# Kernel optimization log

Hardware: AMD Instinct MI355X
Metric: run time of the kernel (lower is better)

## Reference

```python
import jax, jax.numpy as jnp
import numpy as np

B, S_SRC, S_TGT = 32, 64, 1024
D, H, DFF, LE, LD, V = 128, 8, 512, 6, 6, 64


def _pe(S, d):
    # PyTorch-style sinusoidal positional encoding, shape [S, d]
    pos = np.arange(S, dtype=np.float32)[:, None]
    div = np.exp(np.arange(0, d, 2, dtype=np.float32) * (-np.log(10000.0) / d))
    pe = np.zeros((S, d), dtype=np.float32)
    pe[:, 0::2] = np.sin(pos * div)
    pe[:, 1::2] = np.cos(pos * div)
    return jnp.asarray(pe)


def _ln(x, g, b, eps=1e-5):
    m = x.mean(-1, keepdims=True)
    v = ((x - m) ** 2).mean(-1, keepdims=True)
    return (x - m) / jnp.sqrt(v + eps) * g + b


def _mha(q_in, k_in, v_in, Wqkv, bqkv, Wo, bo):
    d = q_in.shape[-1]
    dh = d // H
    def proj(x, W, b):
        return (x @ W.T + b).reshape(x.shape[0], x.shape[1], H, dh)
    q = proj(q_in, Wqkv[:d], bqkv[:d])
    k = proj(k_in, Wqkv[d:2 * d], bqkv[d:2 * d])
    v = proj(v_in, Wqkv[2 * d:], bqkv[2 * d:])
    scores = jnp.einsum('bqhd,bkhd->bhqk', q, k) * (1.0 / np.sqrt(dh))
    a = jax.nn.softmax(scores, axis=-1)
    o = jnp.einsum('bhqk,bkhd->bqhd', a, v).reshape(q_in.shape[0], q_in.shape[1], d)
    return o @ Wo.T + bo


def _ffn(x, W1, b1, W2, b2):
    return jax.nn.relu(x @ W1.T + b1) @ W2.T + b2


def reference(src, tgt, emb,
              enc_qkv_w, enc_qkv_b, enc_out_w, enc_out_b,
              enc_ln1_g, enc_ln1_b, enc_ff1_w, enc_ff1_b,
              enc_ff2_w, enc_ff2_b, enc_ln2_g, enc_ln2_b,
              enc_norm_g, enc_norm_b,
              dec_sa_qkv_w, dec_sa_qkv_b, dec_sa_out_w, dec_sa_out_b,
              dec_ln1_g, dec_ln1_b,
              dec_ca_qkv_w, dec_ca_qkv_b, dec_ca_out_w, dec_ca_out_b,
              dec_ln2_g, dec_ln2_b,
              dec_ff1_w, dec_ff1_b, dec_ff2_w, dec_ff2_b,
              dec_ln3_g, dec_ln3_b, dec_norm_g, dec_norm_b,
              fc_w, fc_b):
    # src: [B, S_SRC] int tokens (occupation config); tgt: [B, S_TGT, D] (zeros in the original)
    s = emb[src] * np.sqrt(float(D)) + _pe(src.shape[1], D)
    t = tgt + _pe(tgt.shape[1], D)
    # encoder (post-norm, ReLU, dropout=0 in eval)
    for i in range(LE):
        s = _ln(s + _mha(s, s, s, enc_qkv_w[i], enc_qkv_b[i], enc_out_w[i], enc_out_b[i]),
                enc_ln1_g[i], enc_ln1_b[i])
        s = _ln(s + _ffn(s, enc_ff1_w[i], enc_ff1_b[i], enc_ff2_w[i], enc_ff2_b[i]),
                enc_ln2_g[i], enc_ln2_b[i])
    mem = _ln(s, enc_norm_g, enc_norm_b)
    # decoder
    for i in range(LD):
        t = _ln(t + _mha(t, t, t, dec_sa_qkv_w[i], dec_sa_qkv_b[i], dec_sa_out_w[i], dec_sa_out_b[i]),
                dec_ln1_g[i], dec_ln1_b[i])
        t = _ln(t + _mha(t, mem, mem, dec_ca_qkv_w[i], dec_ca_qkv_b[i], dec_ca_out_w[i], dec_ca_out_b[i]),
                dec_ln2_g[i], dec_ln2_b[i])
        t = _ln(t + _ffn(t, dec_ff1_w[i], dec_ff1_b[i], dec_ff2_w[i], dec_ff2_b[i]),
                dec_ln3_g[i], dec_ln3_b[i])
    t = _ln(t, dec_norm_g, dec_norm_b)
    return t @ fc_w.T + fc_b  # [B, S_TGT, 1] transformer correction to TN params


def setup_inputs():
    ks = iter(jax.random.split(jax.random.key(0), 64))
    def nrm(shape, scale=0.02):
        return jax.random.normal(next(ks), shape, dtype=jnp.float32) * scale
    inp = {
        'src': jax.random.randint(next(ks), (B, S_SRC), 0, V),
        'tgt': jnp.zeros((B, S_TGT, D), jnp.float32),
        'emb': nrm((V, D), 1.0),
        'enc_qkv_w': nrm((LE, 3 * D, D)), 'enc_qkv_b': jnp.zeros((LE, 3 * D)),
        'enc_out_w': nrm((LE, D, D)), 'enc_out_b': jnp.zeros((LE, D)),
        'enc_ln1_g': jnp.ones((LE, D)), 'enc_ln1_b': jnp.zeros((LE, D)),
        'enc_ff1_w': nrm((LE, DFF, D)), 'enc_ff1_b': jnp.zeros((LE, DFF)),
        'enc_ff2_w': nrm((LE, D, DFF)), 'enc_ff2_b': jnp.zeros((LE, D)),
        'enc_ln2_g': jnp.ones((LE, D)), 'enc_ln2_b': jnp.zeros((LE, D)),
        'enc_norm_g': jnp.ones((D,)), 'enc_norm_b': jnp.zeros((D,)),
        'dec_sa_qkv_w': nrm((LD, 3 * D, D)), 'dec_sa_qkv_b': jnp.zeros((LD, 3 * D)),
        'dec_sa_out_w': nrm((LD, D, D)), 'dec_sa_out_b': jnp.zeros((LD, D)),
        'dec_ln1_g': jnp.ones((LD, D)), 'dec_ln1_b': jnp.zeros((LD, D)),
        'dec_ca_qkv_w': nrm((LD, 3 * D, D)), 'dec_ca_qkv_b': jnp.zeros((LD, 3 * D)),
        'dec_ca_out_w': nrm((LD, D, D)), 'dec_ca_out_b': jnp.zeros((LD, D)),
        'dec_ln2_g': jnp.ones((LD, D)), 'dec_ln2_b': jnp.zeros((LD, D)),
        'dec_ff1_w': nrm((LD, DFF, D)), 'dec_ff1_b': jnp.zeros((LD, DFF)),
        'dec_ff2_w': nrm((LD, D, DFF)), 'dec_ff2_b': jnp.zeros((LD, D)),
        'dec_ln3_g': jnp.ones((LD, D)), 'dec_ln3_b': jnp.zeros((LD, D)),
        'dec_norm_g': jnp.ones((D,)), 'dec_norm_b': jnp.zeros((D,)),
        'fc_w': nrm((1, D)), 'fc_b': jnp.zeros((1,)),
    }
    return inp
```

## Files before the change

kernel.cpp:

```cpp
#include <hip/hip_runtime.h>
#include <hip/hip_bf16.h>
#include <stdint.h>

#define NH 8

typedef uint16_t u16;
typedef uint32_t u32;
typedef __attribute__((ext_vector_type(8))) short s8b;
typedef __attribute__((ext_vector_type(4))) float f32x4;
typedef __attribute__((ext_vector_type(16))) float f32x16;

#if __has_builtin(__builtin_amdgcn_exp2f)
#define EXPS(x) __builtin_amdgcn_exp2f(x)
#define QSCALE 0.36067376022224085f
#else
#define EXPS(x) __expf(x)
#define QSCALE 0.25f
#endif

__device__ __forceinline__ u16 f2b(float f) {
    u32 u = __builtin_bit_cast(u32, f);
    u = (u + 0x7fffu + ((u >> 16) & 1u)) >> 16;
    return (u16)u;
}

__device__ __forceinline__ u32 pkbf(float a, float b) {
    u32 ua = __builtin_bit_cast(u32, a) + 0x8000u;
    u32 ub = __builtin_bit_cast(u32, b) + 0x8000u;
    return __builtin_amdgcn_perm(ub, ua, 0x07060302);
}

__device__ __forceinline__ float pe_val(int pos, int d) {
    int j = d >> 1;
    float div = expf((float)j * -0.14391156831212787f);
    float ang = (float)pos * div;
    return (d & 1) ? cosf(ang) : sinf(ang);
}

__global__ void embed_kernel(const int* __restrict__ src, const float* __restrict__ emb,
                             float* __restrict__ S, u16* __restrict__ Sb) {
    int idx = blockIdx.x * 256 + threadIdx.x;
    int d = idx & 127;
    int n = idx >> 7;
    int i = n & 63;
    int tok = src[n];
    float v = emb[tok * 128 + d] * 11.313708498984761f + pe_val(i, d);
    S[idx] = v; Sb[idx] = f2b(v);
}

__global__ void addpe_kernel(const float* __restrict__ tgt, float* __restrict__ T,
                             u16* __restrict__ Tb) {
    int idx = blockIdx.x * 256 + threadIdx.x;
    int d = idx & 127;
    int n = idx >> 7;
    int i = n & 1023;
    float v = tgt[idx] + pe_val(i, d);
    T[idx] = v; Tb[idx] = f2b(v);
}

struct CvtJobs { const float* src[10]; u16* dst[10]; int n[10]; };
__global__ void cvt_kernel(CvtJobs jb) {
    int e = blockIdx.y;
    int i = blockIdx.x * 256 + threadIdx.x;
    if (i < jb.n[e]) jb.dst[e][i] = f2b(jb.src[e][i]);
}

template <int AI, int BJ, int WM, int WN, int RELU>
__global__ __launch_bounds__(64 * WM * WN) void gemm_direct(
    const u16* __restrict__ A, const u16* __restrict__ W,
    const float* __restrict__ bias, u16* __restrict__ C,
    int M, int N, int K, float qscale, int qcols,
    u16* __restrict__ vt, int vcol0, int sshift, int smask, int skv) {
    int tid = threadIdx.x;
    int lane = tid & 63, w = tid >> 6;
    int quad = lane >> 4, l15 = lane & 15;
    int wmi = w % WM, wni = w / WM;
    int m0 = blockIdx.y * (16 * AI * WM), n0 = blockIdx.x * (16 * BJ * WN);
    int mb = m0 + wmi * 16 * AI, nb = n0 + wni * 16 * BJ;

    const u16* Ab = A + (size_t)(mb + l15) * K + quad * 8;
    const u16* Wb = W + (size_t)(nb + l15) * K + quad * 8;

    f32x4 acc[AI][BJ];
#pragma unroll
    for (int i = 0; i < AI; i++)
#pragma unroll
        for (int j = 0; j < BJ; j++)
#pragma unroll
            for (int r = 0; r < 4; r++) acc[i][j][r] = 0.f;

#pragma unroll 2
    for (int k0 = 0; k0 < K; k0 += 32) {
        s8b af[AI], bf[BJ];
#pragma unroll
        for (int i = 0; i < AI; i++) af[i] = *(const s8b*)(Ab + (size_t)16 * i * K + k0);
#pragma unroll
        for (int j = 0; j < BJ; j++) bf[j] = *(const s8b*)(Wb + (size_t)16 * j * K + k0);
#pragma unroll
        for (int i = 0; i < AI; i++)
#pragma unroll
            for (int j = 0; j < BJ; j++)
                acc[i][j] = __builtin_amdgcn_mfma_f32_16x16x32_bf16(af[i], bf[j], acc[i][j], 0, 0, 0);
    }

    if (vt && n0 == vcol0) {
#pragma unroll
        for (int j = 0; j < BJ; j++) {
            int lc = wni * 16 * BJ + 16 * j + l15;
            int h = lc >> 4, n = lc & 15;
            float bv = bias[vcol0 + lc];
#pragma unroll
            for (int i = 0; i < AI; i++) {
                int row = mb + 16 * i + quad * 4;
                int b = row >> sshift, tok = row & smask;
                u32 lo = pkbf(acc[i][j][0] + bv, acc[i][j][1] + bv);
                u32 hi = pkbf(acc[i][j][2] + bv, acc[i][j][3] + bv);
                u32* p = (u32*)(vt + ((size_t)((b * 8 + h) * 16 + n)) * skv + tok);
                p[0] = lo; p[1] = hi;
            }
        }
        return;
    }
#pragma unroll
    for (int j = 0; j < BJ; j++) {
        int col = nb + 16 * j + l15;
        float bv = bias[col];
        float sc = (col < qcols) ? qscale : 1.f;
#pragma unroll
        for (int i = 0; i < AI; i++) {
            int rbase = mb + 16 * i + quad * 4;
#pragma unroll
            for (int r = 0; r < 4; r++) {
                float v = (acc[i][j][r] + bv) * sc;
                if (RELU) v = fmaxf(v, 0.f);
                C[(size_t)(rbase + r) * N + col] = f2b(v);
            }
        }
    }
}

template <int AI, int BJ, int WM, int WN>
__global__ __launch_bounds__(64 * WM * WN) void gemm_ln_t(
    const u16* __restrict__ A, const u16* __restrict__ W,
    const float* __restrict__ bias, const float* __restrict__ X,
    const float* __restrict__ g, const float* __restrict__ bta,
    float* __restrict__ Y, u16* __restrict__ Yb, int M, int K) {
    __shared__ float redS[16 * AI * WM][WN], redQ[16 * AI * WM][WN];
    int tid = threadIdx.x;
    int lane = tid & 63, w = tid >> 6;
    int quad = lane >> 4, l15 = lane & 15;
    int wmi = w % WM, wni = w / WM;
    int m0 = blockIdx.x * (16 * AI * WM);
    int mb = m0 + wmi * 16 * AI, nb = wni * 16 * BJ;

    const u16* Ab = A + (size_t)(mb + l15) * K + quad * 8;
    const u16* Wb = W + (size_t)(nb + l15) * K + quad * 8;

    f32x4 acc[AI][BJ];
#pragma unroll
    for (int i = 0; i < AI; i++)
#pragma unroll
        for (int j = 0; j < BJ; j++)
#pragma unroll
            for (int r = 0; r < 4; r++) acc[i][j][r] = 0.f;

#pragma unroll 2
    for (int k0 = 0; k0 < K; k0 += 32) {
        s8b af[AI], bf[BJ];
#pragma unroll
        for (int i = 0; i < AI; i++) af[i] = *(const s8b*)(Ab + (size_t)16 * i * K + k0);
#pragma unroll
        for (int j = 0; j < BJ; j++) bf[j] = *(const s8b*)(Wb + (size_t)16 * j * K + k0);
#pragma unroll
        for (int i = 0; i < AI; i++)
#pragma unroll
            for (int j = 0; j < BJ; j++)
                acc[i][j] = __builtin_amdgcn_mfma_f32_16x16x32_bf16(af[i], bf[j], acc[i][j], 0, 0, 0);
    }

#pragma unroll
    for (int i = 0; i < AI; i++)
#pragma unroll
        for (int r = 0; r < 4; r++) {
            int row = mb + 16 * i + quad * 4 + r;
            float s = 0.f, q = 0.f;
#pragma unroll
            for (int j = 0; j < BJ; j++) {
                int col = nb + 16 * j + l15;
                float x = acc[i][j][r] + bias[col] + X[(size_t)row * 128 + col];
                acc[i][j][r] = x;
                s += x; q += x * x;
            }
#pragma unroll
            for (int off = 1; off < 16; off <<= 1) {
                s += __shfl_xor(s, off);
                q += __shfl_xor(q, off);
            }
            if (l15 == 0) {
                int lrow = wmi * 16 * AI + 16 * i + quad * 4 + r;
                redS[lrow][wni] = s;
                redQ[lrow][wni] = q;
            }
        }
    __syncthreads();
#pragma unroll
    for (int i = 0; i < AI; i++)
#pragma unroll
        for (int r = 0; r < 4; r++) {
            int lrow = wmi * 16 * AI + 16 * i + quad * 4 + r;
            int row = m0 + lrow;
            float S2 = 0.f, Q2 = 0.f;
#pragma unroll
            for (int u = 0; u < WN; u++) { S2 += redS[lrow][u]; Q2 += redQ[lrow][u]; }
            float mean = S2 * (1.f / 128.f);
            float var = Q2 * (1.f / 128.f) - mean * mean;
            float rstd = rsqrtf(var + 1e-5f);
#pragma unroll
            for (int j = 0; j < BJ; j++) {
                int col = nb + 16 * j + l15;
                float y = (acc[i][j][r] - mean) * rstd * g[col] + bta[col];
                Y[(size_t)row * 128 + col] = y;
                Yb[(size_t)row * 128 + col] = f2b(y);
            }
        }
}

template <int WAVES>
__global__ __launch_bounds__(WAVES * 64) void attn3(
    const u16* __restrict__ Qb, int qstride, int qoff,
    const u16* __restrict__ Kb, int kstride, int koff,
    const u16* __restrict__ VT,
    u16* __restrict__ O, int SQ, int SKV) {
    __shared__ __align__(16) u32 Ps[WAVES][32 * 20];
    int tid = threadIdx.x;
    int lane = tid & 63, w = tid >> 6;
    int quad = lane >> 4, l15 = lane & 15, l31 = lane & 31, half = lane >> 5;
    int nqc = SQ / (WAVES * 32);
    int bid = blockIdx.x;
    int qc = bid % nqc;
    int h = (bid / nqc) % NH;
    int b = bid / (nqc * NH);
    int q0 = qc * WAVES * 32 + w * 32;

    const u16* qp = Qb + (size_t)(b * SQ + q0 + l31) * qstride + qoff + h * 16 + half * 8;
    s8b qf = *(const s8b*)qp;
    s8b ones;
#pragma unroll
    for (int j = 0; j < 8; j++) ones[j] = (short)0x3F80;

    const u16* vtb = VT + ((size_t)(b * NH + h) * 16 + l15) * SKV + quad * 8;
    const u16* kp = Kb + (size_t)(b * SKV + l31) * kstride + koff + h * 16 + half * 8;
    size_t kadv = (size_t)32 * kstride;

    f32x4 O0, O1, L0, L1;
#pragma unroll
    for (int r = 0; r < 4; r++) { O0[r] = 0.f; O1[r] = 0.f; L0[r] = 0.f; L1[r] = 0.f; }

    u32* pw = Ps[w];
#pragma unroll 2
    for (int j0 = 0; j0 < SKV; j0 += 32) {
        s8b kf = *(const s8b*)kp;
        kp += kadv;
        s8b vb = *(const s8b*)(vtb + j0);
        f32x16 S;
#pragma unroll
        for (int r = 0; r < 16; r++) S[r] = 0.f;
        S = __builtin_amdgcn_mfma_f32_32x32x16_bf16(kf, qf, S, 0, 0, 0);
#pragma unroll
        for (int g = 0; g < 4; g++) {
            float p0 = EXPS(S[4 * g + 0]);
            float p1 = EXPS(S[4 * g + 1]);
            float p2 = EXPS(S[4 * g + 2]);
            float p3 = EXPS(S[4 * g + 3]);
            int kw = l31 * 20 + 2 * half + 4 * g;
            pw[kw] = pkbf(p0, p1);
            pw[kw + 1] = pkbf(p2, p3);
        }
        __builtin_amdgcn_wave_barrier();
        s8b pa0 = *(const s8b*)(pw + l15 * 20 + quad * 4);
        s8b pa1 = *(const s8b*)(pw + (16 + l15) * 20 + quad * 4);
        O0 = __builtin_amdgcn_mfma_f32_16x16x32_bf16(pa0, vb, O0, 0, 0, 0);
        O1 = __builtin_amdgcn_mfma_f32_16x16x32_bf16(pa1, vb, O1, 0, 0, 0);
        L0 = __builtin_amdgcn_mfma_f32_16x16x32_bf16(pa0, ones, L0, 0, 0, 0);
        L1 = __builtin_amdgcn_mfma_f32_16x16x32_bf16(pa1, ones, L1, 0, 0, 0);
    }
#pragma unroll
    for (int r = 0; r < 4; r++) {
        int q = b * SQ + q0 + quad * 4 + r;
        O[(size_t)q * 128 + h * 16 + l15] = f2b(O0[r] / L0[r]);
        O[(size_t)(q + 16) * 128 + h * 16 + l15] = f2b(O1[r] / L1[r]);
    }
}

__global__ void ln_kernel(const float* __restrict__ X, const float* __restrict__ R,
                          const float* __restrict__ g, const float* __restrict__ bta,
                          float* __restrict__ Y, u16* __restrict__ Yb) {
    int r = blockIdx.x;
    int lane = threadIdx.x;
    size_t base = (size_t)r * 128;
    float x0 = X[base + lane], x1 = X[base + lane + 64];
    if (R) { x0 += R[base + lane]; x1 += R[base + lane + 64]; }
    float s = x0 + x1;
    for (int off = 32; off; off >>= 1) s += __shfl_xor(s, off);
    float mean = s * (1.f / 128.f);
    float d0 = x0 - mean, d1 = x1 - mean;
    float vs = d0 * d0 + d1 * d1;
    for (int off = 32; off; off >>= 1) vs += __shfl_xor(vs, off);
    float rstd = rsqrtf(vs * (1.f / 128.f) + 1e-5f);
    float y0 = d0 * rstd * g[lane] + bta[lane];
    float y1 = d1 * rstd * g[lane + 64] + bta[lane + 64];
    Y[base + lane] = y0;
    Y[base + lane + 64] = y1;
    if (Yb) { Yb[base + lane] = f2b(y0); Yb[base + lane + 64] = f2b(y1); }
}

__global__ void fc_kernel(const float* __restrict__ X, const float* __restrict__ w,
                          const float* __restrict__ b, float* __restrict__ out) {
    int r = blockIdx.x;
    int lane = threadIdx.x;
    size_t base = (size_t)r * 128;
    float s = X[base + lane] * w[lane] + X[base + lane + 64] * w[lane + 64];
    for (int off = 32; off; off >>= 1) s += __shfl_xor(s, off);
    if (lane == 0) out[r] = s + b[0];
}

static inline void gemmD(const u16* A, const u16* W, const float* bias, u16* C,
                         int M, int N, int K, hipStream_t st, int qcols = 0,
                         u16* vt = nullptr, int vcol0 = 0, int sshift = 0, int skv = 0) {
    hipLaunchKernelGGL((gemm_direct<4, 4, 2, 2, 0>), dim3(N / 128, M / 128), dim3(256), 0, st,
                       A, W, bias, C, M, N, K, QSCALE, qcols, vt, vcol0, sshift, (1 << sshift) - 1, skv);
}
static inline void gemmDr(const u16* A, const u16* W, const float* bias, u16* C,
                          int M, int N, int K, hipStream_t st) {
    hipLaunchKernelGGL((gemm_direct<4, 4, 2, 2, 1>), dim3(N / 128, M / 128), dim3(256), 0, st,
                       A, W, bias, C, M, N, K, 1.f, 0, (u16*)nullptr, 0, 0, 0, 0);
}
static inline void gemmE(const u16* A, const u16* W, const float* bias, u16* C,
                         int M, int N, int K, hipStream_t st, int qcols = 0,
                         u16* vt = nullptr, int vcol0 = 0, int sshift = 0, int skv = 0) {
    hipLaunchKernelGGL((gemm_direct<2, 2, 1, 4, 0>), dim3(N / 128, M / 32), dim3(256), 0, st,
                       A, W, bias, C, M, N, K, QSCALE, qcols, vt, vcol0, sshift, (1 << sshift) - 1, skv);
}
static inline void gemmEr(const u16* A, const u16* W, const float* bias, u16* C,
                          int M, int N, int K, hipStream_t st) {
    hipLaunchKernelGGL((gemm_direct<2, 2, 1, 4, 1>), dim3(N / 128, M / 32), dim3(256), 0, st,
                       A, W, bias, C, M, N, K, 1.f, 0, (u16*)nullptr, 0, 0, 0, 0);
}
static inline void gemmlnD(const u16* A, const u16* W, const float* bias,
                           const float* X, const float* g, const float* bta,
                           float* Y, u16* Yb, int M, int K, hipStream_t st) {
    hipLaunchKernelGGL((gemm_ln_t<4, 4, 2, 2>), dim3(M / 128), dim3(256), 0, st,
                       A, W, bias, X, g, bta, Y, Yb, M, K);
}
static inline void gemmlnE(const u16* A, const u16* W, const float* bias,
                           const float* X, const float* g, const float* bta,
                           float* Y, u16* Yb, int M, int K, hipStream_t st) {
    hipLaunchKernelGGL((gemm_ln_t<2, 2, 1, 4>), dim3(M / 32), dim3(256), 0, st,
                       A, W, bias, X, g, bta, Y, Yb, M, K);
}

extern "C" void kernel_launch(void* const* d_in, const int* in_sizes, int n_in,
                              void* d_out, int out_size, void* d_ws, size_t ws_size,
                              hipStream_t stream) {
    const int B = 32, SSRC = 64, STGT = 1024, D = 128, DFF_ = 512, LE = 6, LD = 6;

    const int*   src = (const int*)d_in[0];
    const float* tgt = (const float*)d_in[1];
    const float* emb = (const float*)d_in[2];
    const float* enc_qkv_w = (const float*)d_in[3];
    const float* enc_qkv_b = (const float*)d_in[4];
    const float* enc_out_w = (const float*)d_in[5];
    const float* enc_out_b = (const float*)d_in[6];
    const float* enc_ln1_g = (const float*)d_in[7];
    const float* enc_ln1_b = (const float*)d_in[8];
    const float* enc_ff1_w = (const float*)d_in[9];
    const float* enc_ff1_b = (const float*)d_in[10];
    const float* enc_ff2_w = (const float*)d_in[11];
    const float* enc_ff2_b = (const float*)d_in[12];
    const float* enc_ln2_g = (const float*)d_in[13];
    const float* enc_ln2_b = (const float*)d_in[14];
    const float* enc_norm_g = (const float*)d_in[15];
    const float* enc_norm_b = (const float*)d_in[16];
    const float* dec_sa_qkv_w = (const float*)d_in[17];
    const float* dec_sa_qkv_b = (const float*)d_in[18];
    const float* dec_sa_out_w = (const float*)d_in[19];
    const float* dec_sa_out_b = (const float*)d_in[20];
    const float* dec_ln1_g = (const float*)d_in[21];
    const float* dec_ln1_b = (const float*)d_in[22];
    const float* dec_ca_qkv_w = (const float*)d_in[23];
    const float* dec_ca_qkv_b = (const float*)d_in[24];
    const float* dec_ca_out_w = (const float*)d_in[25];
    const float* dec_ca_out_b = (const float*)d_in[26];
    const float* dec_ln2_g = (const float*)d_in[27];
    const float* dec_ln2_b = (const float*)d_in[28];
    const float* dec_ff1_w = (const float*)d_in[29];
    const float* dec_ff1_b = (const float*)d_in[30];
    const float* dec_ff2_w = (const float*)d_in[31];
    const float* dec_ff2_b = (const float*)d_in[32];
    const float* dec_ln3_g = (const float*)d_in[33];
    const float* dec_ln3_b = (const float*)d_in[34];
    const float* dec_norm_g = (const float*)d_in[35];
    const float* dec_norm_b = (const float*)d_in[36];
    const float* fc_w = (const float*)d_in[37];
    const float* fc_b = (const float*)d_in[38];

    const int NT = B * STGT;
    const int NS = B * SSRC;

    float* t_f   = (float*)d_ws;
    float* s_f   = t_f + (size_t)NT * D;
    float* mem_f = s_f + (size_t)NS * D;
    u16* t_bf    = (u16*)(mem_f + (size_t)NS * D);
    u16* s_bf    = t_bf + (size_t)NT * D;
    u16* mem_bf  = s_bf + (size_t)NS * D;
    u16* qkv_bf  = mem_bf + (size_t)NS * D;
    u16* attno_bf = qkv_bf + (size_t)NT * DFF_;
    u16* ckv_bf  = attno_bf + (size_t)NT * D;
    u16* vt      = ckv_bf + (size_t)NS * 2 * D;
    u16* wa      = vt + (size_t)B * NH * 16 * STGT;

    u16* w_enc_qkv = wa;                          int n_enc_qkv = LE * 3 * D * D;
    u16* w_enc_out = w_enc_qkv + n_enc_qkv;       int n_enc_out = LE * D * D;
    u16* w_enc_ff1 = w_enc_out + n_enc_out;       int n_enc_ff1 = LE * DFF_ * D;
    u16* w_enc_ff2 = w_enc_ff1 + n_enc_ff1;       int n_enc_ff2 = LE * D * DFF_;
    u16* w_sa_qkv  = w_enc_ff2 + n_enc_ff2;       int n_sa_qkv = LD * 3 * D * D;
    u16* w_sa_out  = w_sa_qkv + n_sa_qkv;         int n_sa_out = LD * D * D;
    u16* w_ca_qkv  = w_sa_out + n_sa_out;         int n_ca_qkv = LD * 3 * D * D;
    u16* w_ca_out  = w_ca_qkv + n_ca_qkv;         int n_ca_out = LD * D * D;
    u16* w_ff1     = w_ca_out + n_ca_out;         int n_ff1 = LD * DFF_ * D;
    u16* w_ff2     = w_ff1 + n_ff1;               int n_ff2 = LD * D * DFF_;

    float* scf = (float*)qkv_bf;

    CvtJobs jb;
    jb.src[0] = enc_qkv_w;    jb.dst[0] = w_enc_qkv; jb.n[0] = n_enc_qkv;
    jb.src[1] = enc_out_w;    jb.dst[1] = w_enc_out; jb.n[1] = n_enc_out;
    jb.src[2] = enc_ff1_w;    jb.dst[2] = w_enc_ff1; jb.n[2] = n_enc_ff1;
    jb.src[3] = enc_ff2_w;    jb.dst[3] = w_enc_ff2; jb.n[3] = n_enc_ff2;
    jb.src[4] = dec_sa_qkv_w; jb.dst[4] = w_sa_qkv;  jb.n[4] = n_sa_qkv;
    jb.src[5] = dec_sa_out_w; jb.dst[5] = w_sa_out;  jb.n[5] = n_sa_out;
    jb.src[6] = dec_ca_qkv_w; jb.dst[6] = w_ca_qkv;  jb.n[6] = n_ca_qkv;
    jb.src[7] = dec_ca_out_w; jb.dst[7] = w_ca_out;  jb.n[7] = n_ca_out;
    jb.src[8] = dec_ff1_w;    jb.dst[8] = w_ff1;     jb.n[8] = n_ff1;
    jb.src[9] = dec_ff2_w;    jb.dst[9] = w_ff2;     jb.n[9] = n_ff2;
    int maxn = n_enc_ff1;
    hipLaunchKernelGGL(cvt_kernel, dim3((maxn + 255) / 256, 10), dim3(256), 0, stream, jb);

    hipLaunchKernelGGL(embed_kernel, dim3(NS * D / 256), dim3(256), 0, stream, src, emb, s_f, s_bf);

    for (int i = 0; i < LE; i++) {
        gemmE(s_bf, w_enc_qkv + (size_t)i * 3 * D * D, enc_qkv_b + (size_t)i * 3 * D,
              qkv_bf, NS, 3 * D, D, stream, 128, vt, 256, 6, SSRC);
        hipLaunchKernelGGL((attn3<2>), dim3(B * NH), dim3(128), 0, stream,
                           qkv_bf, 3 * D, 0, qkv_bf, 3 * D, D, vt, attno_bf, SSRC, SSRC);
        gemmlnE(attno_bf, w_enc_out + (size_t)i * D * D, enc_out_b + (size_t)i * D,
                s_f, enc_ln1_g + (size_t)i * D, enc_ln1_b + (size_t)i * D, s_f, s_bf, NS, D, stream);
        gemmEr(s_bf, w_enc_ff1 + (size_t)i * DFF_ * D, enc_ff1_b + (size_t)i * DFF_,
               qkv_bf, NS, DFF_, D, stream);
        gemmlnE(qkv_bf, w_enc_ff2 + (size_t)i * D * DFF_, enc_ff2_b + (size_t)i * D,
                s_f, enc_ln2_g + (size_t)i * D, enc_ln2_b + (size_t)i * D, s_f, s_bf, NS, DFF_, stream);
    }
    hipLaunchKernelGGL(ln_kernel, dim3(NS), dim3(64), 0, stream,
                       s_f, (const float*)nullptr, enc_norm_g, enc_norm_b, mem_f, mem_bf);

    hipLaunchKernelGGL(addpe_kernel, dim3(NT * D / 256), dim3(256), 0, stream, tgt, t_f, t_bf);

    for (int i = 0; i < LD; i++) {
        gemmD(t_bf, w_sa_qkv + (size_t)i * 3 * D * D, dec_sa_qkv_b + (size_t)i * 3 * D,
              qkv_bf, NT, 3 * D, D, stream, 128, vt, 256, 10, STGT);
        hipLaunchKernelGGL((attn3<4>), dim3(B * NH * (STGT / 128)), dim3(256), 0, stream,
                           qkv_bf, 3 * D, 0, qkv_bf, 3 * D, D, vt, attno_bf, STGT, STGT);
        gemmlnD(attno_bf, w_sa_out + (size_t)i * D * D, dec_sa_out_b + (size_t)i * D,
                t_f, dec_ln1_g + (size_t)i * D, dec_ln1_b + (size_t)i * D, t_f, t_bf, NT, D, stream);

        gemmD(t_bf, w_ca_qkv + (size_t)i * 3 * D * D, dec_ca_qkv_b + (size_t)i * 3 * D,
              qkv_bf, NT, D, D, stream, 128);
        gemmE(mem_bf, w_ca_qkv + (size_t)i * 3 * D * D + (size_t)D * D,
              dec_ca_qkv_b + (size_t)i * 3 * D + D, ckv_bf, NS, 2 * D, D, stream,
              0, vt, 128, 6, SSRC);
        hipLaunchKernelGGL((attn3<4>), dim3(B * NH * (STGT / 128)), dim3(256), 0, stream,
                           qkv_bf, D, 0, ckv_bf, 2 * D, 0, vt, attno_bf, STGT, SSRC);
        gemmlnD(attno_bf, w_ca_out + (size_t)i * D * D, dec_ca_out_b + (size_t)i * D,
                t_f, dec_ln2_g + (size_t)i * D, dec_ln2_b + (size_t)i * D, t_f, t_bf, NT, D, stream);

        gemmDr(t_bf, w_ff1 + (size_t)i * DFF_ * D, dec_ff1_b + (size_t)i * DFF_,
               qkv_bf, NT, DFF_, D, stream);
        gemmlnD(qkv_bf, w_ff2 + (size_t)i * D * DFF_, dec_ff2_b + (size_t)i * D,
                t_f, dec_ln3_g + (size_t)i * D, dec_ln3_b + (size_t)i * D, t_f, t_bf, NT, DFF_, stream);
    }

    hipLaunchKernelGGL(ln_kernel, dim3(NT), dim3(64), 0, stream,
                       t_f, (const float*)nullptr, dec_norm_g, dec_norm_b, scf, (u16*)nullptr);
    hipLaunchKernelGGL(fc_kernel, dim3(NT), dim3(64), 0, stream,
                       scf, fc_w, fc_b, (float*)d_out);
}
```

Baseline: 1.552 ms.

## Rewrite attention to keep P in registers and drop fp32 residual stream

```diff
diff --git a/kernel.cpp b/kernel.cpp
--- a/kernel.cpp
+++ b/kernel.cpp
@@ -7,6 +7,7 @@
 typedef uint16_t u16;
 typedef uint32_t u32;
 typedef __attribute__((ext_vector_type(8))) short s8b;
+typedef __attribute__((ext_vector_type(4))) u32 u32x4;
 typedef __attribute__((ext_vector_type(4))) float f32x4;
 typedef __attribute__((ext_vector_type(16))) float f32x16;
 
@@ -23,7 +24,9 @@
     u = (u + 0x7fffu + ((u >> 16) & 1u)) >> 16;
     return (u16)u;
 }
-
+__device__ __forceinline__ float b2f(u16 u) {
+    return __builtin_bit_cast(float, (u32)u << 16);
+}
 __device__ __forceinline__ u32 pkbf(float a, float b) {
     u32 ua = __builtin_bit_cast(u32, a) + 0x8000u;
     u32 ub = __builtin_bit_cast(u32, b) + 0x8000u;
@@ -38,24 +41,21 @@
 }
 
 __global__ void embed_kernel(const int* __restrict__ src, const float* __restrict__ emb,
-                             float* __restrict__ S, u16* __restrict__ Sb) {
+                             u16* __restrict__ Sb) {
     int idx = blockIdx.x * 256 + threadIdx.x;
     int d = idx & 127;
     int n = idx >> 7;
     int i = n & 63;
     int tok = src[n];
-    float v = emb[tok * 128 + d] * 11.313708498984761f + pe_val(i, d);
-    S[idx] = v; Sb[idx] = f2b(v);
-}
-
-__global__ void addpe_kernel(const float* __restrict__ tgt, float* __restrict__ T,
-                             u16* __restrict__ Tb) {
+    Sb[idx] = f2b(emb[tok * 128 + d] * 11.313708498984761f + pe_val(i, d));
+}
+
+__global__ void addpe_kernel(const float* __restrict__ tgt, u16* __restrict__ Tb) {
     int idx = blockIdx.x * 256 + threadIdx.x;
     int d = idx & 127;
     int n = idx >> 7;
     int i = n & 1023;
-    float v = tgt[idx] + pe_val(i, d);
-    T[idx] = v; Tb[idx] = f2b(v);
+    Tb[idx] = f2b(tgt[idx] + pe_val(i, d));
 }
 
 struct CvtJobs { const float* src[10]; u16* dst[10]; int n[10]; };
@@ -142,9 +142,9 @@
 template <int AI, int BJ, int WM, int WN>
 __global__ __launch_bounds__(64 * WM * WN) void gemm_ln_t(
     const u16* __restrict__ A, const u16* __restrict__ W,
-    const float* __restrict__ bias, const float* __restrict__ X,
+    const float* __restrict__ bias, const u16* __restrict__ X,
     const float* __restrict__ g, const float* __restrict__ bta,
-    float* __restrict__ Y, u16* __restrict__ Yb, int M, int K) {
+    u16* __restrict__ Yb, int M, int K) {
     __shared__ float redS[16 * AI * WM][WN], redQ[16 * AI * WM][WN];
     int tid = threadIdx.x;
     int lane = tid & 63, w = tid >> 6;
@@ -187,7 +187,7 @@
 #pragma unroll
             for (int j = 0; j < BJ; j++) {
                 int col = nb + 16 * j + l15;
-                float x = acc[i][j][r] + bias[col] + X[(size_t)row * 128 + col];
+                float x = acc[i][j][r] + bias[col] + b2f(X[(size_t)row * 128 + col]);
                 acc[i][j][r] = x;
                 s += x; q += x * x;
             }
@@ -219,87 +219,79 @@
             for (int j = 0; j < BJ; j++) {
                 int col = nb + 16 * j + l15;
                 float y = (acc[i][j][r] - mean) * rstd * g[col] + bta[col];
-                Y[(size_t)row * 128 + col] = y;
                 Yb[(size_t)row * 128 + col] = f2b(y);
             }
         }
 }
 
 template <int WAVES>
-__global__ __launch_bounds__(WAVES * 64) void attn3(
-    const u16* __restrict__ Qb, int qstride, int qoff,
+__global__ __launch_bounds__(WAVES * 64) void attn4(
+    const u16* __restrict__ Qb, int qstride,
     const u16* __restrict__ Kb, int kstride, int koff,
     const u16* __restrict__ VT,
     u16* __restrict__ O, int SQ, int SKV) {
-    __shared__ __align__(16) u32 Ps[WAVES][32 * 20];
     int tid = threadIdx.x;
     int lane = tid & 63, w = tid >> 6;
-    int quad = lane >> 4, l15 = lane & 15, l31 = lane & 31, half = lane >> 5;
-    int nqc = SQ / (WAVES * 32);
+    int l31 = lane & 31, half = lane >> 5;
     int bid = blockIdx.x;
-    int qc = bid % nqc;
-    int h = (bid / nqc) % NH;
-    int b = bid / (nqc * NH);
-    int q0 = qc * WAVES * 32 + w * 32;
-
-    const u16* qp = Qb + (size_t)(b * SQ + q0 + l31) * qstride + qoff + h * 16 + half * 8;
+    int bh = bid & 255;
+    int qc = bid >> 8;
+    int h = bh & 7, b = bh >> 3;
+    int q0 = qc * (WAVES * 32) + w * 32;
+
+    int ksw = (l31 & 19) | ((l31 & 4) << 1) | ((l31 & 8) >> 1);
+
+    const u16* qp = Qb + (size_t)(b * SQ + q0 + l31) * qstride + h * 16 + half * 8;
     s8b qf = *(const s8b*)qp;
-    s8b ones;
-#pragma unroll
-    for (int j = 0; j < 8; j++) ones[j] = (short)0x3F80;
-
-    const u16* vtb = VT + ((size_t)(b * NH + h) * 16 + l15) * SKV + quad * 8;
-    const u16* kp = Kb + (size_t)(b * SKV + l31) * kstride + koff + h * 16 + half * 8;
+    const u16* kp = Kb + (size_t)(b * SKV + ksw) * kstride + koff + h * 16 + half * 8;
     size_t kadv = (size_t)32 * kstride;
-
-    f32x4 O0, O1, L0, L1;
-#pragma unroll
-    for (int r = 0; r < 4; r++) { O0[r] = 0.f; O1[r] = 0.f; L0[r] = 0.f; L1[r] = 0.f; }
-
-    u32* pw = Ps[w];
+    const u16* va = VT + (size_t)(bh * 16 + l31) * SKV + half * 8;
+
+    f32x16 Oa;
+#pragma unroll
+    for (int r = 0; r < 16; r++) Oa[r] = 0.f;
+    float lsum = 0.f;
+
 #pragma unroll 2
     for (int j0 = 0; j0 < SKV; j0 += 32) {
         s8b kf = *(const s8b*)kp;
         kp += kadv;
-        s8b vb = *(const s8b*)(vtb + j0);
+        s8b v1 = *(const s8b*)(va + j0);
+        s8b v2 = *(const s8b*)(va + j0 + 16);
         f32x16 S;
 #pragma unroll
         for (int r = 0; r < 16; r++) S[r] = 0.f;
         S = __builtin_amdgcn_mfma_f32_32x32x16_bf16(kf, qf, S, 0, 0, 0);
-#pragma unroll
-        for (int g = 0; g < 4; g++) {
-            float p0 = EXPS(S[4 * g + 0]);
-            float p1 = EXPS(S[4 * g + 1]);
-            float p2 = EXPS(S[4 * g + 2]);
-            float p3 = EXPS(S[4 * g + 3]);
-            int kw = l31 * 20 + 2 * half + 4 * g;
-            pw[kw] = pkbf(p0, p1);
-            pw[kw + 1] = pkbf(p2, p3);
-        }
-        __builtin_amdgcn_wave_barrier();
-        s8b pa0 = *(const s8b*)(pw + l15 * 20 + quad * 4);
-        s8b pa1 = *(const s8b*)(pw + (16 + l15) * 20 + quad * 4);
-        O0 = __builtin_amdgcn_mfma_f32_16x16x32_bf16(pa0, vb, O0, 0, 0, 0);
-        O1 = __builtin_amdgcn_mfma_f32_16x16x32_bf16(pa1, vb, O1, 0, 0, 0);
-        L0 = __builtin_amdgcn_mfma_f32_16x16x32_bf16(pa0, ones, L0, 0, 0, 0);
-        L1 = __builtin_amdgcn_mfma_f32_16x16x32_bf16(pa1, ones, L1, 0, 0, 0);
-    }
-#pragma unroll
-    for (int r = 0; r < 4; r++) {
-        int q = b * SQ + q0 + quad * 4 + r;
-        O[(size_t)q * 128 + h * 16 + l15] = f2b(O0[r] / L0[r]);
-        O[(size_t)(q + 16) * 128 + h * 16 + l15] = f2b(O1[r] / L1[r]);
-    }
-}
-
-__global__ void ln_kernel(const float* __restrict__ X, const float* __restrict__ R,
-                          const float* __restrict__ g, const float* __restrict__ bta,
-                          float* __restrict__ Y, u16* __restrict__ Yb) {
+        float e[16];
+#pragma unroll
+        for (int r = 0; r < 16; r++) { e[r] = EXPS(S[r]); lsum += e[r]; }
+        u32x4 p1, p2;
+        p1[0] = pkbf(e[0], e[1]);  p1[1] = pkbf(e[2], e[3]);
+        p1[2] = pkbf(e[4], e[5]);  p1[3] = pkbf(e[6], e[7]);
+        p2[0] = pkbf(e[8], e[9]);  p2[1] = pkbf(e[10], e[11]);
+        p2[2] = pkbf(e[12], e[13]); p2[3] = pkbf(e[14], e[15]);
+        s8b B1 = __builtin_bit_cast(s8b, p1);
+        s8b B2 = __builtin_bit_cast(s8b, p2);
+        Oa = __builtin_amdgcn_mfma_f32_32x32x16_bf16(v1, B1, Oa, 0, 0, 0);
+        Oa = __builtin_amdgcn_mfma_f32_32x32x16_bf16(v2, B2, Oa, 0, 0, 0);
+    }
+    lsum += __shfl_xor(lsum, 32);
+    float inv = 1.f / lsum;
+    int q = b * SQ + q0 + l31;
+    u16* op = O + (size_t)q * 128 + h * 16 + 4 * half;
+    ((u32*)op)[0] = pkbf(Oa[0] * inv, Oa[1] * inv);
+    ((u32*)op)[1] = pkbf(Oa[2] * inv, Oa[3] * inv);
+    ((u32*)(op + 8))[0] = pkbf(Oa[4] * inv, Oa[5] * inv);
+    ((u32*)(op + 8))[1] = pkbf(Oa[6] * inv, Oa[7] * inv);
+}
+
+__global__ void ln_bf(const u16* __restrict__ X,
+                      const float* __restrict__ g, const float* __restrict__ bta,
+                      float* __restrict__ Yf, u16* __restrict__ Yb) {
     int r = blockIdx.x;
     int lane = threadIdx.x;
     size_t base = (size_t)r * 128;
-    float x0 = X[base + lane], x1 = X[base + lane + 64];
-    if (R) { x0 += R[base + lane]; x1 += R[base + lane + 64]; }
+    float x0 = b2f(X[base + lane]), x1 = b2f(X[base + lane + 64]);
     float s = x0 + x1;
     for (int off = 32; off; off >>= 1) s += __shfl_xor(s, off);
     float mean = s * (1.f / 128.f);
@@ -309,8 +301,7 @@
     float rstd = rsqrtf(vs * (1.f / 128.f) + 1e-5f);
     float y0 = d0 * rstd * g[lane] + bta[lane];
     float y1 = d1 * rstd * g[lane + 64] + bta[lane + 64];
-    Y[base + lane] = y0;
-    Y[base + lane + 64] = y1;
+    if (Yf) { Yf[base + lane] = y0; Yf[base + lane + 64] = y1; }
     if (Yb) { Yb[base + lane] = f2b(y0); Yb[base + lane + 64] = f2b(y1); }
 }
 
@@ -347,16 +338,16 @@
                        A, W, bias, C, M, N, K, 1.f, 0, (u16*)nullptr, 0, 0, 0, 0);
 }
 static inline void gemmlnD(const u16* A, const u16* W, const float* bias,
-                           const float* X, const float* g, const float* bta,
-                           float* Y, u16* Yb, int M, int K, hipStream_t st) {
+                           const u16* X, const float* g, const float* bta,
+                           u16* Yb, int M, int K, hipStream_t st) {
     hipLaunchKernelGGL((gemm_ln_t<4, 4, 2, 2>), dim3(M / 128), dim3(256), 0, st,
-                       A, W, bias, X, g, bta, Y, Yb, M, K);
+                       A, W, bias, X, g, bta, Yb, M, K);
 }
 static inline void gemmlnE(const u16* A, const u16* W, const float* bias,
-                           const float* X, const float* g, const float* bta,
-                           float* Y, u16* Yb, int M, int K, hipStream_t st) {
+                           const u16* X, const float* g, const float* bta,
+                           u16* Yb, int M, int K, hipStream_t st) {
     hipLaunchKernelGGL((gemm_ln_t<2, 2, 1, 4>), dim3(M / 32), dim3(256), 0, st,
-                       A, W, bias, X, g, bta, Y, Yb, M, K);
+                       A, W, bias, X, g, bta, Yb, M, K);
 }
 
 extern "C" void kernel_launch(void* const* d_in, const int* in_sizes, int n_in,
@@ -407,17 +398,14 @@
     const int NT = B * STGT;
     const int NS = B * SSRC;
 
-    float* t_f   = (float*)d_ws;
-    float* s_f   = t_f + (size_t)NT * D;
-    float* mem_f = s_f + (size_t)NS * D;
-    u16* t_bf    = (u16*)(mem_f + (size_t)NS * D);
+    u16* t_bf    = (u16*)d_ws;
     u16* s_bf    = t_bf + (size_t)NT * D;
     u16* mem_bf  = s_bf + (size_t)NS * D;
     u16* qkv_bf  = mem_bf + (size_t)NS * D;
     u16* attno_bf = qkv_bf + (size_t)NT * DFF_;
     u16* ckv_bf  = attno_bf + (size_t)NT * D;
     u16* vt      = ckv_bf + (size_t)NS * 2 * D;
-    u16* wa      = vt + (size_t)B * NH * 16 * STGT;
+    u16* wa      = vt + (size_t)B * NH * 16 * STGT + 16 * STGT;
 
     u16* w_enc_qkv = wa;                          int n_enc_qkv = LE * 3 * D * D;
     u16* w_enc_out = w_enc_qkv + n_enc_qkv;       int n_enc_out = LE * D * D;
@@ -446,51 +434,51 @@
     int maxn = n_enc_ff1;
     hipLaunchKernelGGL(cvt_kernel, dim3((maxn + 255) / 256, 10), dim3(256), 0, stream, jb);
 
-    hipLaunchKernelGGL(embed_kernel, dim3(NS * D / 256), dim3(256), 0, stream, src, emb, s_f, s_bf);
+    hipLaunchKernelGGL(embed_kernel, dim3(NS * D / 256), dim3(256), 0, stream, src, emb, s_bf);
 
     for (int i = 0; i < LE; i++) {
         gemmE(s_bf, w_enc_qkv + (size_t)i * 3 * D * D, enc_qkv_b + (size_t)i * 3 * D,
               qkv_bf, NS, 3 * D, D, stream, 128, vt, 256, 6, SSRC);
-        hipLaunchKernelGGL((attn3<2>), dim3(B * NH), dim3(128), 0, stream,
-                           qkv_bf, 3 * D, 0, qkv_bf, 3 * D, D, vt, attno_bf, SSRC, SSRC);
+        hipLaunchKernelGGL((attn4<2>), dim3(256), dim3(128), 0, stream,
+                           qkv_bf, 3 * D, qkv_bf, 3 * D, D, vt, attno_bf, SSRC, SSRC);
         gemmlnE(attno_bf, w_enc_out + (size_t)i * D * D, enc_out_b + (size_t)i * D,
-                s_f, enc_ln1_g + (size_t)i * D, enc_ln1_b + (size_t)i * D, s_f, s_bf, NS, D, stream);
+                s_bf, enc_ln1_g + (size_t)i * D, enc_ln1_b + (size_t)i * D, s_bf, NS, D, stream);
         gemmEr(s_bf, w_enc_ff1 + (size_t)i * DFF_ * D, enc_ff1_b + (size_t)i * DFF_,
                qkv_bf, NS, DFF_, D, stream);
         gemmlnE(qkv_bf, w_enc_ff2 + (size_t)i * D * DFF_, enc_ff2_b + (size_t)i * D,
-                s_f, enc_ln2_g + (size_t)i * D, enc_ln2_b + (size_t)i * D, s_f, s_bf, NS, DFF_, stream);
-    }
-    hipLaunchKernelGGL(ln_kernel, dim3(NS), dim3(64), 0, stream,
-                       s_f, (const float*)nullptr, enc_norm_g, enc_norm_b, mem_f, mem_bf);
-
-    hipLaunchKernelGGL(addpe_kernel, dim3(NT * D / 256), dim3(256), 0, stream, tgt, t_f, t_bf);
+                s_bf, enc_ln2_g + (size_t)i * D, enc_ln2_b + (size_t)i * D, s_bf, NS, DFF_, stream);
+    }
+    hipLaunchKernelGGL(ln_bf, dim3(NS), dim3(64), 0, stream,
+                       s_bf, enc_norm_g, enc_norm_b, (float*)nullptr, mem_bf);
+
+    hipLaunchKernelGGL(addpe_kernel, dim3(NT * D / 256), dim3(256), 0, stream, tgt, t_bf);
 
     for (int i = 0; i < LD; i++) {
         gemmD(t_bf, w_sa_qkv + (size_t)i * 3 * D * D, dec_sa_qkv_b + (size_t)i * 3 * D,
               qkv_bf, NT, 3 * D, D, stream, 128, vt, 256, 10, STGT);
-        hipLaunchKernelGGL((attn3<4>), dim3(B * NH * (STGT / 128)), dim3(256), 0, stream,
-                           qkv_bf, 3 * D, 0, qkv_bf, 3 * D, D, vt, attno_bf, STGT, STGT);
+        hipLaunchKernelGGL((attn4<4>), dim3(8 * 256), dim3(256), 0, stream,
+                           qkv_bf, 3 * D, qkv_bf, 3 * D, D, vt, attno_bf, STGT, STGT);
         gemmlnD(attno_bf, w_sa_out + (size_t)i * D * D, dec_sa_out_b + (size_t)i * D,
-                t_f, dec_ln1_g + (size_t)i * D, dec_ln1_b + (size_t)i * D, t_f, t_bf, NT, D, stream);
+                t_bf, dec_ln1_g + (size_t)i * D, dec_ln1_b + (size_t)i * D, t_bf, NT, D, stream);
 
         gemmD(t_bf, w_ca_qkv + (size_t)i * 3 * D * D, dec_ca_qkv_b + (size_t)i * 3 * D,
               qkv_bf, NT, D, D, stream, 128);
         gemmE(mem_bf, w_ca_qkv + (size_t)i * 3 * D * D + (size_t)D * D,
               dec_ca_qkv_b + (size_t)i * 3 * D + D, ckv_bf, NS, 2 * D, D, stream,
               0, vt, 128, 6, SSRC);
-        hipLaunchKernelGGL((attn3<4>), dim3(B * NH * (STGT / 128)), dim3(256), 0, stream,
-                           qkv_bf, D, 0, ckv_bf, 2 * D, 0, vt, attno_bf, STGT, SSRC);
+        hipLaunchKernelGGL((attn4<4>), dim3(8 * 256), dim3(256), 0, stream,
+                           qkv_bf, D, ckv_bf, 2 * D, 0, vt, attno_bf, STGT, SSRC);
         gemmlnD(attno_bf, w_ca_out + (size_t)i * D * D, dec_ca_out_b + (size_t)i * D,
-                t_f, dec_ln2_g + (size_t)i * D, dec_ln2_b + (size_t)i * D, t_f, t_bf, NT, D, stream);
+                t_bf, dec_ln2_g + (size_t)i * D, dec_ln2_b + (size_t)i * D, t_bf, NT, D, stream);
 
         gemmDr(t_bf, w_ff1 + (size_t)i * DFF_ * D, dec_ff1_b + (size_t)i * DFF_,
                qkv_bf, NT, DFF_, D, stream);
         gemmlnD(qkv_bf, w_ff2 + (size_t)i * D * DFF_, dec_ff2_b + (size_t)i * D,
-                t_f, dec_ln3_g + (size_t)i * D, dec_ln3_b + (size_t)i * D, t_f, t_bf, NT, DFF_, stream);
-    }
-
-    hipLaunchKernelGGL(ln_kernel, dim3(NT), dim3(64), 0, stream,
-                       t_f, (const float*)nullptr, dec_norm_g, dec_norm_b, scf, (u16*)nullptr);
+                t_bf, dec_ln3_g + (size_t)i * D, dec_ln3_b + (size_t)i * D, t_bf, NT, DFF_, stream);
+    }
+
+    hipLaunchKernelGGL(ln_bf, dim3(NT), dim3(64), 0, stream,
+                       t_bf, dec_norm_g, dec_norm_b, scf, (u16*)nullptr);
     hipLaunchKernelGGL(fc_kernel, dim3(NT), dim3(64), 0, stream,
                        scf, fc_w, fc_b, (float*)d_out);
 }
```

Result: slower. 1.921 ms (+23.8%).
